# Performance work log

Hardware: AMD Instinct MI355X
Metric: run time of the kernel (lower is better)

## Reference

```python
import jax, jax.numpy as jnp
import numpy as np
from jax import lax

RATIO = 0.25
K = 32


def setup_inputs() -> dict:
    key = jax.random.key(0)
    ks = jax.random.split(key, 5)
    B, N, C = 16, 4096, 64
    pos = jax.random.normal(ks[0], (B, N, 3), jnp.float32)
    x = jax.random.normal(ks[1], (B, N, C), jnp.float32)

    def lin(k, fan_in, fan_out):
        return jax.random.normal(k, (fan_in, fan_out), jnp.float32) / np.sqrt(fan_in).astype(np.float32)

    W1 = lin(ks[2], C + 3, 128); b1 = jnp.zeros((128,), jnp.float32)
    W2 = lin(ks[3], 128, 128);   b2 = jnp.zeros((128,), jnp.float32)
    W3 = lin(ks[4], 128, 256);   b3 = jnp.zeros((256,), jnp.float32)
    return dict(x=x, pos=pos, W1=W1, b1=b1, W2=W2, b2=b2, W3=W3, b3=b3)


def _fps(pos, M):
    """Iterative farthest point sampling on one cloud. pos: [N,3] -> idx [M]."""
    N = pos.shape[0]

    def step(carry, _):
        dists, last = carry
        d = jnp.sum((pos - pos[last]) ** 2, axis=-1)      # [N]
        dists = jnp.minimum(dists, d)
        nxt = jnp.argmax(dists).astype(jnp.int32)
        return (dists, nxt), last

    init = (jnp.full((N,), 1e30, pos.dtype), jnp.int32(0))
    _, idx = lax.scan(step, init, None, length=M)
    return idx  # first emitted index is 0, then farthest points in order


def reference(x, pos, W1, b1, W2, b2, W3, b3):
    B, N, _ = pos.shape
    M = int(N * RATIO)

    # --- FPS sampling per cloud ---
    idx = jax.vmap(lambda p: _fps(p, M))(pos)                        # [B,M] int32
    pos_s = jnp.take_along_axis(pos, idx[..., None], axis=1)          # [B,M,3]

    # --- kNN graph: K nearest source points for each sampled centroid ---
    d2 = jnp.sum((pos_s[:, :, None, :] - pos[:, None, :, :]) ** 2, -1)  # [B,M,N]
    _, nidx = lax.top_k(-d2, K)                                       # [B,M,K]

    # --- gather neighbor features & relative positions ---
    x_j = jax.vmap(lambda xb, ib: xb[ib])(x, nidx)                    # [B,M,K,C]
    pos_j = jax.vmap(lambda pb, ib: pb[ib])(pos, nidx)                # [B,M,K,3]
    rel = pos_j - pos_s[:, :, None, :]                                # [B,M,K,3]

    # --- PointNetConv: local MLP on [x_j || rel], max aggregation ---
    msg = jnp.concatenate([x_j, rel], axis=-1)                        # [B,M,K,C+3]
    h = jax.nn.relu(msg @ W1 + b1)
    h = jax.nn.relu(h @ W2 + b2)
    h = jax.nn.relu(h @ W3 + b3)                                      # [B,M,K,256]
    out = jnp.max(h, axis=2)                                          # [B,M,256]
    return out, pos_s
```

## Files before the change

### kernel.cpp

```cpp
#include <hip/hip_runtime.h>


#define B_    16
#define N_    4096
#define M_    1024
#define AST   136
#define NWORK 240
#define NITEM (256 * 16)

typedef __bf16 bf16x8 __attribute__((ext_vector_type(8)));
typedef __bf16 bf16x4 __attribute__((ext_vector_type(4)));
typedef float  f32x4  __attribute__((ext_vector_type(4)));
typedef float  f32x2  __attribute__((ext_vector_type(2)));

__global__ __launch_bounds__(256) void prep_weights(
    const float* __restrict__ W1, const float* __restrict__ W2,
    const float* __restrict__ W3,
    __bf16* __restrict__ w1t, __bf16* __restrict__ w2t, __bf16* __restrict__ w3t) {
  const int t = blockIdx.x * 256 + threadIdx.x;
  if (t < 128 * 96) {
    const int n = t / 96, k = t % 96;
    w1t[t] = (k < 67) ? (__bf16)W1[k * 128 + n] : (__bf16)0.0f;
  }
  if (t < 128 * 128) {
    const int n = t >> 7, k = t & 127;
    w2t[t] = (__bf16)W2[k * 128 + n];
  }
  {
    const int n = t >> 7, k = t & 127;
    w3t[t] = (__bf16)W3[k * 256 + n];
  }
}

__device__ __forceinline__ f32x2 pk_sub(f32x2 a, f32x2 b) {
  f32x2 d;
  asm("v_pk_add_f32 %0, %1, %2 neg_lo:[0,1] neg_hi:[0,1]" : "=v"(d) : "v"(a), "v"(b));
  return d;
}
__device__ __forceinline__ f32x2 pk_mul(f32x2 a, f32x2 b) {
  f32x2 d;
  asm("v_pk_mul_f32 %0, %1, %2" : "=v"(d) : "v"(a), "v"(b));
  return d;
}
__device__ __forceinline__ f32x2 pk_add(f32x2 a, f32x2 b) {
  f32x2 d;
  asm("v_pk_add_f32 %0, %1, %2" : "=v"(d) : "v"(a), "v"(b));
  return d;
}

template <int CTRL>
__device__ __forceinline__ unsigned long long dpp_max_u64(unsigned long long k) {
  unsigned lo = (unsigned)__builtin_amdgcn_update_dpp(0, (int)(unsigned)k,         CTRL, 0xF, 0xF, true);
  unsigned hi = (unsigned)__builtin_amdgcn_update_dpp(0, (int)(unsigned)(k >> 32), CTRL, 0xF, 0xF, true);
  unsigned long long p = ((unsigned long long)hi << 32) | lo;
  return p > k ? p : k;
}

union ShU {
  struct { float4 pp[N_]; unsigned long long sw[2][4]; } f;
  struct { __bf16 A[128 * AST]; __bf16 Bv[128 * AST]; } g;
};

__global__ __launch_bounds__(256) void fused_kernel(
    const float* __restrict__ pos, const float* __restrict__ x,
    const float* __restrict__ b1, const float* __restrict__ b2,
    const float* __restrict__ b3,
    const __bf16* __restrict__ w1t, const __bf16* __restrict__ w2t,
    const __bf16* __restrict__ w3t,
    int* __restrict__ ipub, int* __restrict__ ctr,
    float* __restrict__ out, float* __restrict__ pos_s) {
  __shared__ alignas(16) ShU sh;
  __shared__ int sh_item;
  const int tid = threadIdx.x;

  if (blockIdx.x < B_) {
    __builtin_amdgcn_s_setprio(3);
    const int b = blockIdx.x;
    const float* pb = pos + (size_t)b * N_ * 3;
    for (int i = tid; i < N_; i += 256)
      sh.f.pp[i] = make_float4(pb[3 * i], pb[3 * i + 1], pb[3 * i + 2], 0.0f);
    __syncthreads();

    f32x2 X2[8], Y2[8], Z2[8];
    float D[16];
    unsigned lo16[16];
    const unsigned ntid = ~(unsigned)tid;
#pragma unroll
    for (int j = 0; j < 8; j++) {
      float4 p0 = sh.f.pp[tid + ((2 * j) << 8)];
      float4 p1 = sh.f.pp[tid + ((2 * j + 1) << 8)];
      X2[j][0] = p0.x; X2[j][1] = p1.x;
      Y2[j][0] = p0.y; Y2[j][1] = p1.y;
      Z2[j][0] = p0.z; Z2[j][1] = p1.z;
      D[2 * j] = 1e30f; D[2 * j + 1] = 1e30f;
      lo16[2 * j]     = ntid - (unsigned)((2 * j) << 8);
      lo16[2 * j + 1] = ntid - (unsigned)((2 * j + 1) << 8);
    }

    float4 q = sh.f.pp[0];
    if (tid == 0) {
      __hip_atomic_store(ipub + b * M_, 1, __ATOMIC_RELAXED,
                         __HIP_MEMORY_SCOPE_AGENT);
      float* o = pos_s + (size_t)b * M_ * 3;
      o[0] = q.x; o[1] = q.y; o[2] = q.z;
    }

    for (int i = 1; i < M_; i++) {
      f32x2 qx; qx[0] = q.x; qx[1] = q.x;
      f32x2 qy; qy[0] = q.y; qy[1] = q.y;
      f32x2 qz; qz[0] = q.z; qz[1] = q.z;
      unsigned long long key[16];
#pragma unroll
      for (int j = 0; j < 8; j++) {
        f32x2 dx = pk_sub(X2[j], qx);
        f32x2 dy = pk_sub(Y2[j], qy);
        f32x2 dz = pk_sub(Z2[j], qz);
        f32x2 t0 = pk_mul(dx, dx);
        f32x2 t1 = pk_mul(dy, dy);
        f32x2 s  = pk_add(t0, t1);
        f32x2 t2 = pk_mul(dz, dz);
        f32x2 d2 = pk_add(s, t2);
        D[2 * j]     = fminf(D[2 * j],     d2[0]);
        D[2 * j + 1] = fminf(D[2 * j + 1], d2[1]);
        key[2 * j]     = ((unsigned long long)__float_as_uint(D[2 * j])     << 32) | lo16[2 * j];
        key[2 * j + 1] = ((unsigned long long)__float_as_uint(D[2 * j + 1]) << 32) | lo16[2 * j + 1];
      }
#pragma unroll
      for (int s = 8; s > 0; s >>= 1)
#pragma unroll
        for (int k = 0; k < s; k++)
          if (key[k + s] > key[k]) key[k] = key[k + s];
      unsigned long long kk = key[0];

      kk = dpp_max_u64<0xB1>(kk);
      kk = dpp_max_u64<0x4E>(kk);
      kk = dpp_max_u64<0x141>(kk);
      kk = dpp_max_u64<0x140>(kk);
      kk = dpp_max_u64<0x142>(kk);
      kk = dpp_max_u64<0x143>(kk);

      const int par = i & 1;
      if ((tid & 63) == 63) sh.f.sw[par][tid >> 6] = kk;
      __syncthreads();

      const ulonglong2 v01 = *(const ulonglong2*)&sh.f.sw[par][0];
      const ulonglong2 v23 = *(const ulonglong2*)&sh.f.sw[par][2];
      const int c0 = (int)(~(unsigned)v01.x), c1 = (int)(~(unsigned)v01.y);
      const int c2 = (int)(~(unsigned)v23.x), c3 = (int)(~(unsigned)v23.y);
      float4 q0 = sh.f.pp[c0], q1 = sh.f.pp[c1], q2 = sh.f.pp[c2], q3 = sh.f.pp[c3];
      unsigned long long k01, k23; float4 q01, q23; int i01, i23;
      if (v01.y > v01.x) { k01 = v01.y; q01 = q1; i01 = c1; }
      else               { k01 = v01.x; q01 = q0; i01 = c0; }
      if (v23.y > v23.x) { k23 = v23.y; q23 = q3; i23 = c3; }
      else               { k23 = v23.x; q23 = q2; i23 = c2; }
      int cur;
      if (k23 > k01) { q = q23; cur = i23; }
      else           { q = q01; cur = i01; }

      if (tid == 0) {
        __hip_atomic_store(ipub + b * M_ + i, cur + 1, __ATOMIC_RELAXED,
                           __HIP_MEMORY_SCOPE_AGENT);
        float* o = pos_s + ((size_t)b * M_ + i) * 3;
        o[0] = q.x; o[1] = q.y; o[2] = q.z;
      }
    }
    return;
  }

  const int w    = tid >> 6;
  const int lane = tid & 63;

  for (;;) {
    if (tid == 0) sh_item = atomicAdd(ctr, 1);
    __syncthreads();
    const int it = sh_item;
    if (it >= NITEM) return;
    const int b    = it & 15;
    const int mset = it >> 4;
    const int m    = mset * 4 + w;

    __syncthreads();
    {
      const float* pb = pos + (size_t)b * N_ * 3;
      for (int i = tid; i < N_; i += 256)
        sh.f.pp[i] = make_float4(pb[3 * i], pb[3 * i + 1], pb[3 * i + 2], 0.0f);
    }
    __syncthreads();

    int ci0 = 0;
    if (lane == 0) {
      int v;
      while ((v = __hip_atomic_load(ipub + b * M_ + m, __ATOMIC_RELAXED,
                                    __HIP_MEMORY_SCOPE_AGENT)) == 0)
        __builtin_amdgcn_s_sleep(8);
      ci0 = v - 1;
    }
    const int ci = __shfl(ci0, 0);
    const float4 c = sh.f.pp[ci];

    float d2v[64];
    unsigned long long kmin = ~0ull;
#pragma unroll
    for (int t = 0; t < 64; t++) {
      const int j = t * 64 + lane;
      const float4 p = sh.f.pp[j];
      float dx = __fsub_rn(p.x, c.x);
      float dy = __fsub_rn(p.y, c.y);
      float dz = __fsub_rn(p.z, c.z);
      float d  = __fadd_rn(__fadd_rn(__fmul_rn(dx, dx), __fmul_rn(dy, dy)),
                           __fmul_rn(dz, dz));
      d2v[t] = d;
      const unsigned long long k64 =
          ((unsigned long long)__float_as_uint(d) << 32) | (unsigned int)j;
      if (k64 < kmin) kmin = k64;
    }

    unsigned long long sk = kmin;
#pragma unroll
    for (int size = 2; size <= 64; size <<= 1) {
#pragma unroll
      for (int stride = size >> 1; stride > 0; stride >>= 1) {
        const unsigned long long other = __shfl_xor(sk, stride);
        const bool up      = ((lane & size) == 0);
        const bool lowhalf = ((lane & stride) == 0);
        const bool takeMin = (up == lowhalf);
        const bool swp     = takeMin ? (other < sk) : (other > sk);
        if (swp) sk = other;
      }
    }
    const unsigned long long T0 = __shfl(sk, 31);
    const bool seeded = (kmin <= T0);

    unsigned long long rkey = (lane < 32) ? sk : ~0ull;
    unsigned long long wk   = T0;

#pragma unroll
    for (int t = 0; t < 64; t++) {
      const int j = t * 64 + lane;
      const unsigned long long k64 =
          ((unsigned long long)__float_as_uint(d2v[t]) << 32) | (unsigned int)j;
      const bool skip = seeded && (k64 == kmin);
      unsigned long long mask = __ballot((k64 < wk) && !skip);
      if (mask) {
        while (mask) {
          const int src = __ffsll((unsigned long long)mask) - 1;
          mask &= mask - 1;
          const unsigned long long cand = __shfl(k64, src);
          const int pos_i = (int)__popcll(__ballot(rkey < cand));
          const unsigned long long sh_ = __shfl_up(rkey, 1);
          if (lane < 32) {
            if (lane == pos_i)      rkey = cand;
            else if (lane > pos_i)  rkey = sh_;
          }
        }
        wk = __shfl(rkey, 31);
      }
    }
    const int njl = (int)(rkey & 0xFFFFull);
    __syncthreads();

    {
      const int rl   = lane >> 1;
      const int half = lane & 1;
      const int r    = w * 32 + rl;
      const int nj   = __shfl(njl, rl);
      const float4* xr = (const float4*)(x + ((size_t)(b * N_ + nj)) * 64 + half * 32);
      __bf16* dst = &sh.g.A[r * AST + half * 32];
#pragma unroll
      for (int t = 0; t < 8; t++) {
        float4 v = xr[t];
        bf16x4 u;
        u[0] = (__bf16)v.x; u[1] = (__bf16)v.y; u[2] = (__bf16)v.z; u[3] = (__bf16)v.w;
        *(bf16x4*)(dst + t * 4) = u;
      }
      bf16x8 z;
#pragma unroll
      for (int q2 = 0; q2 < 8; q2++) z[q2] = (__bf16)0.0f;
      if (half == 0) {
        const float* pj = pos + ((size_t)(b * N_ + nj)) * 3;
        bf16x8 u = z;
        u[0] = (__bf16)(pj[0] - c.x);
        u[1] = (__bf16)(pj[1] - c.y);
        u[2] = (__bf16)(pj[2] - c.z);
        *(bf16x8*)&sh.g.A[r * AST + 64] = u;
        *(bf16x8*)&sh.g.A[r * AST + 72] = z;
      } else {
        *(bf16x8*)&sh.g.A[r * AST + 80] = z;
        *(bf16x8*)&sh.g.A[r * AST + 88] = z;
      }
    }
    __syncthreads();

    const int lrow = lane & 15;
    const int lk8  = (lane >> 4) << 3;
    const int orow = (lane >> 4) << 2;

    {
      f32x4 acc[8][2];
#pragma unroll
      for (int n = 0; n < 2; n++) {
        const float bv = b1[(2 * w + n) * 16 + lrow];
        f32x4 a = {bv, bv, bv, bv};
#pragma unroll
        for (int rt = 0; rt < 8; rt++) acc[rt][n] = a;
      }
#pragma unroll
      for (int s = 0; s < 3; s++) {
        bf16x8 a[8];
#pragma unroll
        for (int rt = 0; rt < 8; rt++)
          a[rt] = *(const bf16x8*)&sh.g.A[(rt * 16 + lrow) * AST + s * 32 + lk8];
#pragma unroll
        for (int n = 0; n < 2; n++) {
          bf16x8 bb = *(const bf16x8*)&w1t[((2 * w + n) * 16 + lrow) * 96 + s * 32 + lk8];
#pragma unroll
          for (int rt = 0; rt < 8; rt++)
            acc[rt][n] = __builtin_amdgcn_mfma_f32_16x16x32_bf16(a[rt], bb, acc[rt][n], 0, 0, 0);
        }
      }
      __syncthreads();
#pragma unroll
      for (int n = 0; n < 2; n++)
#pragma unroll
        for (int rt = 0; rt < 8; rt++)
#pragma unroll
          for (int j = 0; j < 4; j++)
            sh.g.Bv[(rt * 16 + orow + j) * AST + (2 * w + n) * 16 + lrow] =
                (__bf16)fmaxf(acc[rt][n][j], 0.0f);
    }
    __syncthreads();

    {
      f32x4 acc[8][2];
#pragma unroll
      for (int n = 0; n < 2; n++) {
        const float bv = b2[(2 * w + n) * 16 + lrow];
        f32x4 a = {bv, bv, bv, bv};
#pragma unroll
        for (int rt = 0; rt < 8; rt++) acc[rt][n] = a;
      }
#pragma unroll
      for (int s = 0; s < 4; s++) {
        bf16x8 a[8];
#pragma unroll
        for (int rt = 0; rt < 8; rt++)
          a[rt] = *(const bf16x8*)&sh.g.Bv[(rt * 16 + lrow) * AST + s * 32 + lk8];
#pragma unroll
        for (int n = 0; n < 2; n++) {
          bf16x8 bb = *(const bf16x8*)&w2t[((2 * w + n) * 16 + lrow) * 128 + s * 32 + lk8];
#pragma unroll
          for (int rt = 0; rt < 8; rt++)
            acc[rt][n] = __builtin_amdgcn_mfma_f32_16x16x32_bf16(a[rt], bb, acc[rt][n], 0, 0, 0);
        }
      }
      __syncthreads();
#pragma unroll
      for (int n = 0; n < 2; n++)
#pragma unroll
        for (int rt = 0; rt < 8; rt++)
#pragma unroll
          for (int j = 0; j < 4; j++)
            sh.g.A[(rt * 16 + orow + j) * AST + (2 * w + n) * 16 + lrow] =
                (__bf16)fmaxf(acc[rt][n][j], 0.0f);
    }
    __syncthreads();

#pragma unroll
    for (int np = 0; np < 2; np++) {
      f32x4 acc[8][2];
#pragma unroll
      for (int n = 0; n < 2; n++) {
        const float bv = b3[(4 * w + 2 * np + n) * 16 + lrow];
        f32x4 a = {bv, bv, bv, bv};
#pragma unroll
        for (int rt = 0; rt < 8; rt++) acc[rt][n] = a;
      }
#pragma unroll
      for (int s = 0; s < 4; s++) {
        bf16x8 a[8];
#pragma unroll
        for (int rt = 0; rt < 8; rt++)
          a[rt] = *(const bf16x8*)&sh.g.A[(rt * 16 + lrow) * AST + s * 32 + lk8];
#pragma unroll
        for (int n = 0; n < 2; n++) {
          bf16x8 bb = *(const bf16x8*)&w3t[((4 * w + 2 * np + n) * 16 + lrow) * 128 + s * 32 + lk8];
#pragma unroll
          for (int rt = 0; rt < 8; rt++)
            acc[rt][n] = __builtin_amdgcn_mfma_f32_16x16x32_bf16(a[rt], bb, acc[rt][n], 0, 0, 0);
        }
      }
#pragma unroll
      for (int ccc = 0; ccc < 4; ccc++) {
#pragma unroll
        for (int n = 0; n < 2; n++) {
          f32x4 a0 = acc[2 * ccc][n], a1 = acc[2 * ccc + 1][n];
          float v = fmaxf(fmaxf(fmaxf(a0[0], a0[1]), fmaxf(a0[2], a0[3])),
                          fmaxf(fmaxf(a1[0], a1[1]), fmaxf(a1[2], a1[3])));
          v = fmaxf(v, __shfl_xor(v, 16));
          v = fmaxf(v, __shfl_xor(v, 32));
          v = fmaxf(v, 0.0f);
          if (lane < 16)
            out[((size_t)(b * M_ + mset * 4 + ccc)) * 256 + (4 * w + 2 * np + n) * 16 + lane] = v;
        }
      }
    }
  }
}

extern "C" void kernel_launch(void* const* d_in, const int* in_sizes, int n_in,
                              void* d_out, int out_size, void* d_ws, size_t ws_size,
                              hipStream_t stream) {
  const float* x   = (const float*)d_in[0];
  const float* pos = (const float*)d_in[1];
  const float* W1  = (const float*)d_in[2];
  const float* b1  = (const float*)d_in[3];
  const float* W2  = (const float*)d_in[4];
  const float* b2  = (const float*)d_in[5];
  const float* W3  = (const float*)d_in[6];
  const float* b3  = (const float*)d_in[7];

  float* out   = (float*)d_out;
  float* pos_s = out + (size_t)B_ * M_ * 256;

  char* ws = (char*)d_ws;
  int*    ipub = (int*)ws;
  int*    ctr  = (int*)(ws + 65536);
  __bf16* w1t  = (__bf16*)(ws + 65792);
  __bf16* w2t  = (__bf16*)(ws + 90368);
  __bf16* w3t  = (__bf16*)(ws + 123136);

  hipMemsetAsync(ws, 0, 65540, stream);
  prep_weights<<<dim3(128), dim3(256), 0, stream>>>(W1, W2, W3, w1t, w2t, w3t);
  fused_kernel<<<dim3(B_ + NWORK), dim3(256), 0, stream>>>(
      pos, x, b1, b2, b3, w1t, w2t, w3t, ipub, ctr, out, pos_s);
}
```

Before: 666.5 us.

## Run two FPS clouds per block to halve barrier count per cloud

Each FPS block now processes two point clouds together, interleaving their distance updates and reductions and sharing one __syncthreads per iteration, so only 8 FPS blocks are launched instead of 16. This is meant to amortize the per-iteration barrier and latency of the serial FPS loop across two independent chains, exposing ILP. The cost is doubled per-iteration arithmetic on one block, higher register use, and a larger shared-memory union, and the FPS critical path per block gets longer.

New measurement: 1.255 ms. 88.3% more time.

```diff
diff --git a/kernel.cpp b/kernel.cpp
--- a/kernel.cpp
+++ b/kernel.cpp
@@ -5,6 +5,7 @@
 #define N_    4096
 #define M_    1024
 #define AST   136
+#define NFPSB 8
 #define NWORK 240
 #define NITEM (256 * 16)
 
@@ -57,7 +58,7 @@
 }
 
 union ShU {
-  struct { float4 pp[N_]; unsigned long long sw[2][4]; } f;
+  struct { float4 pp[2][N_]; unsigned long long sw[2][2][4]; } f;
   struct { __bf16 A[128 * AST]; __bf16 Bv[128 * AST]; } g;
 };
 
@@ -73,95 +74,118 @@
   __shared__ int sh_item;
   const int tid = threadIdx.x;
 
-  if (blockIdx.x < B_) {
+  if (blockIdx.x < NFPSB) {
     __builtin_amdgcn_s_setprio(3);
-    const int b = blockIdx.x;
-    const float* pb = pos + (size_t)b * N_ * 3;
-    for (int i = tid; i < N_; i += 256)
-      sh.f.pp[i] = make_float4(pb[3 * i], pb[3 * i + 1], pb[3 * i + 2], 0.0f);
-    __syncthreads();
-
-    f32x2 X2[8], Y2[8], Z2[8];
-    float D[16];
+    const int b0 = blockIdx.x * 2;
+#pragma unroll
+    for (int c = 0; c < 2; c++) {
+      const float* pb = pos + (size_t)(b0 + c) * N_ * 3;
+      for (int i = tid; i < N_; i += 256)
+        sh.f.pp[c][i] = make_float4(pb[3 * i], pb[3 * i + 1], pb[3 * i + 2], 0.0f);
+    }
+    __syncthreads();
+
+    f32x2 X2[2][8], Y2[2][8], Z2[2][8];
+    float D[2][16];
     unsigned lo16[16];
     const unsigned ntid = ~(unsigned)tid;
 #pragma unroll
     for (int j = 0; j < 8; j++) {
-      float4 p0 = sh.f.pp[tid + ((2 * j) << 8)];
-      float4 p1 = sh.f.pp[tid + ((2 * j + 1) << 8)];
-      X2[j][0] = p0.x; X2[j][1] = p1.x;
-      Y2[j][0] = p0.y; Y2[j][1] = p1.y;
-      Z2[j][0] = p0.z; Z2[j][1] = p1.z;
-      D[2 * j] = 1e30f; D[2 * j + 1] = 1e30f;
       lo16[2 * j]     = ntid - (unsigned)((2 * j) << 8);
       lo16[2 * j + 1] = ntid - (unsigned)((2 * j + 1) << 8);
-    }
-
-    float4 q = sh.f.pp[0];
+#pragma unroll
+      for (int c = 0; c < 2; c++) {
+        float4 p0 = sh.f.pp[c][tid + ((2 * j) << 8)];
+        float4 p1 = sh.f.pp[c][tid + ((2 * j + 1) << 8)];
+        X2[c][j][0] = p0.x; X2[c][j][1] = p1.x;
+        Y2[c][j][0] = p0.y; Y2[c][j][1] = p1.y;
+        Z2[c][j][0] = p0.z; Z2[c][j][1] = p1.z;
+        D[c][2 * j] = 1e30f; D[c][2 * j + 1] = 1e30f;
+      }
+    }
+
+    float4 q[2] = { sh.f.pp[0][0], sh.f.pp[1][0] };
     if (tid == 0) {
-      __hip_atomic_store(ipub + b * M_, 1, __ATOMIC_RELAXED,
-                         __HIP_MEMORY_SCOPE_AGENT);
-      float* o = pos_s + (size_t)b * M_ * 3;
-      o[0] = q.x; o[1] = q.y; o[2] = q.z;
+#pragma unroll
+      for (int c = 0; c < 2; c++) {
+        __hip_atomic_store(ipub + (b0 + c) * M_, 1, __ATOMIC_RELAXED,
+                           __HIP_MEMORY_SCOPE_AGENT);
+        float* o = pos_s + (size_t)(b0 + c) * M_ * 3;
+        o[0] = q[c].x; o[1] = q[c].y; o[2] = q[c].z;
+      }
     }
 
     for (int i = 1; i < M_; i++) {
-      f32x2 qx; qx[0] = q.x; qx[1] = q.x;
-      f32x2 qy; qy[0] = q.y; qy[1] = q.y;
-      f32x2 qz; qz[0] = q.z; qz[1] = q.z;
-      unsigned long long key[16];
-#pragma unroll
-      for (int j = 0; j < 8; j++) {
-        f32x2 dx = pk_sub(X2[j], qx);
-        f32x2 dy = pk_sub(Y2[j], qy);
-        f32x2 dz = pk_sub(Z2[j], qz);
-        f32x2 t0 = pk_mul(dx, dx);
-        f32x2 t1 = pk_mul(dy, dy);
-        f32x2 s  = pk_add(t0, t1);
-        f32x2 t2 = pk_mul(dz, dz);
-        f32x2 d2 = pk_add(s, t2);
-        D[2 * j]     = fminf(D[2 * j],     d2[0]);
-        D[2 * j + 1] = fminf(D[2 * j + 1], d2[1]);
-        key[2 * j]     = ((unsigned long long)__float_as_uint(D[2 * j])     << 32) | lo16[2 * j];
-        key[2 * j + 1] = ((unsigned long long)__float_as_uint(D[2 * j + 1]) << 32) | lo16[2 * j + 1];
-      }
-#pragma unroll
-      for (int s = 8; s > 0; s >>= 1)
-#pragma unroll
-        for (int k = 0; k < s; k++)
-          if (key[k + s] > key[k]) key[k] = key[k + s];
-      unsigned long long kk = key[0];
-
-      kk = dpp_max_u64<0xB1>(kk);
-      kk = dpp_max_u64<0x4E>(kk);
-      kk = dpp_max_u64<0x141>(kk);
-      kk = dpp_max_u64<0x140>(kk);
-      kk = dpp_max_u64<0x142>(kk);
-      kk = dpp_max_u64<0x143>(kk);
+      unsigned long long kk[2];
+#pragma unroll
+      for (int c = 0; c < 2; c++) {
+        f32x2 qx; qx[0] = q[c].x; qx[1] = q[c].x;
+        f32x2 qy; qy[0] = q[c].y; qy[1] = q[c].y;
+        f32x2 qz; qz[0] = q[c].z; qz[1] = q[c].z;
+        unsigned long long key[16];
+#pragma unroll
+        for (int j = 0; j < 8; j++) {
+          f32x2 dx = pk_sub(X2[c][j], qx);
+          f32x2 dy = pk_sub(Y2[c][j], qy);
+          f32x2 dz = pk_sub(Z2[c][j], qz);
+          f32x2 t0 = pk_mul(dx, dx);
+          f32x2 t1 = pk_mul(dy, dy);
+          f32x2 s  = pk_add(t0, t1);
+          f32x2 t2 = pk_mul(dz, dz);
+          f32x2 d2 = pk_add(s, t2);
+          D[c][2 * j]     = fminf(D[c][2 * j],     d2[0]);
+          D[c][2 * j + 1] = fminf(D[c][2 * j + 1], d2[1]);
+          key[2 * j]     = ((unsigned long long)__float_as_uint(D[c][2 * j])     << 32) | lo16[2 * j];
+          key[2 * j + 1] = ((unsigned long long)__float_as_uint(D[c][2 * j + 1]) << 32) | lo16[2 * j + 1];
+        }
+#pragma unroll
+        for (int s = 8; s > 0; s >>= 1)
+#pragma unroll
+          for (int k = 0; k < s; k++)
+            if (key[k + s] > key[k]) key[k] = key[k + s];
+        unsigned long long t = key[0];
+        t = dpp_max_u64<0xB1>(t);
+        t = dpp_max_u64<0x4E>(t);
+        t = dpp_max_u64<0x141>(t);
+        t = dpp_max_u64<0x140>(t);
+        t = dpp_max_u64<0x142>(t);
+        t = dpp_max_u64<0x143>(t);
+        kk[c] = t;
+      }
 
       const int par = i & 1;
-      if ((tid & 63) == 63) sh.f.sw[par][tid >> 6] = kk;
+      if ((tid & 63) == 63) {
+        sh.f.sw[0][par][tid >> 6] = kk[0];
+        sh.f.sw[1][par][tid >> 6] = kk[1];
+      }
       __syncthreads();
 
-      const ulonglong2 v01 = *(const ulonglong2*)&sh.f.sw[par][0];
-      const ulonglong2 v23 = *(const ulonglong2*)&sh.f.sw[par][2];
-      const int c0 = (int)(~(unsigned)v01.x), c1 = (int)(~(unsigned)v01.y);
-      const int c2 = (int)(~(unsigned)v23.x), c3 = (int)(~(unsigned)v23.y);
-      float4 q0 = sh.f.pp[c0], q1 = sh.f.pp[c1], q2 = sh.f.pp[c2], q3 = sh.f.pp[c3];
-      unsigned long long k01, k23; float4 q01, q23; int i01, i23;
-      if (v01.y > v01.x) { k01 = v01.y; q01 = q1; i01 = c1; }
-      else               { k01 = v01.x; q01 = q0; i01 = c0; }
-      if (v23.y > v23.x) { k23 = v23.y; q23 = q3; i23 = c3; }
-      else               { k23 = v23.x; q23 = q2; i23 = c2; }
-      int cur;
-      if (k23 > k01) { q = q23; cur = i23; }
-      else           { q = q01; cur = i01; }
+      int cur[2];
+#pragma unroll
+      for (int c = 0; c < 2; c++) {
+        const ulonglong2 v01 = *(const ulonglong2*)&sh.f.sw[c][par][0];
+        const ulonglong2 v23 = *(const ulonglong2*)&sh.f.sw[c][par][2];
+        const int c0 = (int)(~(unsigned)v01.x), c1 = (int)(~(unsigned)v01.y);
+        const int c2 = (int)(~(unsigned)v23.x), c3 = (int)(~(unsigned)v23.y);
+        float4 q0 = sh.f.pp[c][c0], q1 = sh.f.pp[c][c1];
+        float4 q2 = sh.f.pp[c][c2], q3 = sh.f.pp[c][c3];
+        unsigned long long k01, k23; float4 q01, q23; int i01, i23;
+        if (v01.y > v01.x) { k01 = v01.y; q01 = q1; i01 = c1; }
+        else               { k01 = v01.x; q01 = q0; i01 = c0; }
+        if (v23.y > v23.x) { k23 = v23.y; q23 = q3; i23 = c3; }
+        else               { k23 = v23.x; q23 = q2; i23 = c2; }
+        if (k23 > k01) { q[c] = q23; cur[c] = i23; }
+        else           { q[c] = q01; cur[c] = i01; }
+      }
 
       if (tid == 0) {
-        __hip_atomic_store(ipub + b * M_ + i, cur + 1, __ATOMIC_RELAXED,
-                           __HIP_MEMORY_SCOPE_AGENT);
-        float* o = pos_s + ((size_t)b * M_ + i) * 3;
-        o[0] = q.x; o[1] = q.y; o[2] = q.z;
+#pragma unroll
+        for (int c = 0; c < 2; c++) {
+          __hip_atomic_store(ipub + (b0 + c) * M_ + i, cur[c] + 1, __ATOMIC_RELAXED,
+                             __HIP_MEMORY_SCOPE_AGENT);
+          float* o = pos_s + ((size_t)(b0 + c) * M_ + i) * 3;
+          o[0] = q[c].x; o[1] = q[c].y; o[2] = q[c].z;
+        }
       }
     }
     return;
@@ -183,7 +207,7 @@
     {
       const float* pb = pos + (size_t)b * N_ * 3;
       for (int i = tid; i < N_; i += 256)
-        sh.f.pp[i] = make_float4(pb[3 * i], pb[3 * i + 1], pb[3 * i + 2], 0.0f);
+        sh.f.pp[0][i] = make_float4(pb[3 * i], pb[3 * i + 1], pb[3 * i + 2], 0.0f);
     }
     __syncthreads();
 
@@ -196,14 +220,14 @@
       ci0 = v - 1;
     }
     const int ci = __shfl(ci0, 0);
-    const float4 c = sh.f.pp[ci];
+    const float4 c = sh.f.pp[0][ci];
 
     float d2v[64];
     unsigned long long kmin = ~0ull;
 #pragma unroll
     for (int t = 0; t < 64; t++) {
       const int j = t * 64 + lane;
-      const float4 p = sh.f.pp[j];
+      const float4 p = sh.f.pp[0][j];
       float dx = __fsub_rn(p.x, c.x);
       float dy = __fsub_rn(p.y, c.y);
       float dz = __fsub_rn(p.z, c.z);
@@ -431,6 +455,6 @@
 
   hipMemsetAsync(ws, 0, 65540, stream);
   prep_weights<<<dim3(128), dim3(256), 0, stream>>>(W1, W2, W3, w1t, w2t, w3t);
-  fused_kernel<<<dim3(B_ + NWORK), dim3(256), 0, stream>>>(
+  fused_kernel<<<dim3(NFPSB + NWORK), dim3(256), 0, stream>>>(
       pos, x, b1, b2, b3, w1t, w2t, w3t, ipub, ctr, out, pos_s);
 }
```
